# Kernel tuning notes

Hardware: AMD Instinct MI355X
Metric: run time of the kernel (lower is better)

## Reference

```python
import jax, jax.numpy as jnp
import numpy as np

N = 30000      # num nodes
E = 600000     # num edges
D = 128        # feature dim (all layers)
R = 7          # num_relation
G = 16         # num graphs in batch
L = 3          # num layers (hidden_dims = [128,128,128])


def setup_inputs() -> dict:
    key = jax.random.key(0)
    ks = jax.random.split(key, 10)
    x = jax.random.normal(ks[0], (N, D), dtype=jnp.float32)
    node_in = jax.random.randint(ks[1], (E,), 0, N)
    node_out = jax.random.randint(ks[2], (E,), 0, N)
    relation = jax.random.randint(ks[3], (E,), 0, R)
    edge_weight = jax.random.uniform(ks[4], (E,), dtype=jnp.float32)
    node2graph = jnp.sort(jax.random.randint(ks[5], (N,), 0, G))
    # learned params: per-layer relational linear (R*D -> D) and self-loop linear (D -> D)
    Wr = jax.random.normal(ks[6], (L, R * D, D), dtype=jnp.float32) * 0.02
    br = jnp.zeros((L, D), dtype=jnp.float32)
    Wl = jax.random.normal(ks[7], (L, D, D), dtype=jnp.float32) * 0.02
    bl = jnp.zeros((L, D), dtype=jnp.float32)
    return dict(x=x, node_in=node_in, node_out=node_out, relation=relation,
                edge_weight=edge_weight, node2graph=node2graph,
                Wr=Wr, br=br, Wl=Wl, bl=bl)


def reference(x, node_in, node_out, relation, edge_weight, node2graph, Wr, br, Wl, bl):
    # relation-indexed destination segment: node_out * R + relation
    seg = node_out * R + relation            # (E,)
    ew = edge_weight[:, None]                # (E, 1)
    h = x
    for i in range(L):
        msg = h[node_in] * ew                                         # gather + weight, (E, D)
        upd = jax.ops.segment_sum(msg, seg, num_segments=N * R)       # scatter_add, (N*R, D)
        upd = upd.reshape(N, R * D)                                   # per-relation concat
        h = jax.nn.relu(upd @ Wr[i] + br[i] + h @ Wl[i] + bl[i])      # linear + self-loop + act
    node_feature = h                                                  # (N, D)
    graph_feature = jax.ops.segment_sum(node_feature, node2graph, num_segments=G)  # sum readout
    return graph_feature, node_feature
```

## Files before the change

kernel.cpp:

```cpp
#include <hip/hip_runtime.h>

#define NN 30000
#define NE 600000
#define DD 128
#define RR 7
#define GG 16
#define LL 3

typedef short bf16x8 __attribute__((ext_vector_type(8)));
typedef float f32x4  __attribute__((ext_vector_type(4)));

__device__ __forceinline__ unsigned short f2bf(float f) {
    unsigned u = __float_as_uint(f);
    unsigned r = (u + 0x7fffu + ((u >> 16) & 1u)) >> 16;
    return (unsigned short)r;
}

__global__ __launch_bounds__(256) void pack_weights(
    const float* __restrict__ Wl,
    const float* __restrict__ Wr,
    unsigned short* __restrict__ Bw)
{
    int t = blockIdx.x * 256 + threadIdx.x;
    if (t >= LL * 1024 * DD) return;
    int l = t >> 17;
    int rem = t & 131071;
    int n = rem >> 7;
    int k = rem & 127;
    float v;
    if (n < DD) {
        v = Wl[(size_t)l * DD * DD + k * DD + n];
    } else {
        int q = n - DD;
        v = Wr[(size_t)l * RR * DD * DD + (size_t)((q >> 7) * DD + k) * DD + (q & 127)];
    }
    Bw[(size_t)l * 1024 * DD + n * DD + k] = f2bf(v);
}

__global__ __launch_bounds__(256) void convert_bf16(
    const float* __restrict__ in, unsigned short* __restrict__ out, int n4)
{
    int i = blockIdx.x * 256 + threadIdx.x;
    if (i >= n4) return;
    float4 v = ((const float4*)in)[i];
    ushort4 o;
    o.x = f2bf(v.x); o.y = f2bf(v.y); o.z = f2bf(v.z); o.w = f2bf(v.w);
    ((ushort4*)out)[i] = o;
}

#define ASTR 136
__global__ __launch_bounds__(256) void gemm_mfma(
    const unsigned short* __restrict__ hb,
    const unsigned short* __restrict__ Bw,
    const float* __restrict__ br,
    const float* __restrict__ bl,
    float* __restrict__ hacc,
    unsigned short* __restrict__ Zb,
    int N)
{
    __shared__ unsigned short As[64 * ASTR];
    __shared__ unsigned short Bs[128 * ASTR];

    const int tid  = threadIdx.x;
    const int wave = tid >> 6;
    const int lane = tid & 63;
    const int quad = lane >> 4;
    const int l16  = lane & 15;
    const int row0 = blockIdx.x * 64;
    const int col0 = blockIdx.y * 128;

#pragma unroll
    for (int l = 0; l < 4; ++l) {
        int f = tid + l * 256;
        int r = f >> 4;
        int c8 = f & 15;
        int row = row0 + r;
        int4 v = make_int4(0, 0, 0, 0);
        if (row < N) v = *(const int4*)(hb + (size_t)row * DD + c8 * 8);
        *(int4*)(As + r * ASTR + c8 * 8) = v;
    }
#pragma unroll
    for (int l = 0; l < 8; ++l) {
        int f = tid + l * 256;
        int n = f >> 4;
        int c8 = f & 15;
        *(int4*)(Bs + n * ASTR + c8 * 8) =
            *(const int4*)(Bw + (size_t)(col0 + n) * DD + c8 * 8);
    }
    __syncthreads();

    f32x4 acc[4][2];
#pragma unroll
    for (int mt = 0; mt < 4; ++mt)
#pragma unroll
        for (int nt = 0; nt < 2; ++nt)
            acc[mt][nt] = (f32x4){0.f, 0.f, 0.f, 0.f};

    const unsigned short* As_l = As + l16 * ASTR;
    const unsigned short* Bs_l = Bs + (wave * 32 + l16) * ASTR;

#pragma unroll
    for (int kc = 0; kc < 4; ++kc) {
        int ko = kc * 32 + quad * 8;
        bf16x8 a0 = *(const bf16x8*)(As_l + 0 * 16 * ASTR + ko);
        bf16x8 a1 = *(const bf16x8*)(As_l + 1 * 16 * ASTR + ko);
        bf16x8 a2 = *(const bf16x8*)(As_l + 2 * 16 * ASTR + ko);
        bf16x8 a3 = *(const bf16x8*)(As_l + 3 * 16 * ASTR + ko);
        bf16x8 b0 = *(const bf16x8*)(Bs_l + 0 * 16 * ASTR + ko);
        bf16x8 b1 = *(const bf16x8*)(Bs_l + 1 * 16 * ASTR + ko);
        acc[0][0] = __builtin_amdgcn_mfma_f32_16x16x32_bf16(a0, b0, acc[0][0], 0, 0, 0);
        acc[1][0] = __builtin_amdgcn_mfma_f32_16x16x32_bf16(a1, b0, acc[1][0], 0, 0, 0);
        acc[2][0] = __builtin_amdgcn_mfma_f32_16x16x32_bf16(a2, b0, acc[2][0], 0, 0, 0);
        acc[3][0] = __builtin_amdgcn_mfma_f32_16x16x32_bf16(a3, b0, acc[3][0], 0, 0, 0);
        acc[0][1] = __builtin_amdgcn_mfma_f32_16x16x32_bf16(a0, b1, acc[0][1], 0, 0, 0);
        acc[1][1] = __builtin_amdgcn_mfma_f32_16x16x32_bf16(a1, b1, acc[1][1], 0, 0, 0);
        acc[2][1] = __builtin_amdgcn_mfma_f32_16x16x32_bf16(a2, b1, acc[2][1], 0, 0, 0);
        acc[3][1] = __builtin_amdgcn_mfma_f32_16x16x32_bf16(a3, b1, acc[3][1], 0, 0, 0);
    }

    const int ncol = wave * 32 + l16;
    if (col0 == 0) {
        float bias0 = br[ncol] + bl[ncol];
        float bias1 = br[ncol + 16] + bl[ncol + 16];
#pragma unroll
        for (int mt = 0; mt < 4; ++mt) {
#pragma unroll
            for (int reg = 0; reg < 4; ++reg) {
                int row = row0 + mt * 16 + quad * 4 + reg;
                if (row < N) {
                    hacc[(size_t)row * DD + ncol]      = acc[mt][0][reg] + bias0;
                    hacc[(size_t)row * DD + ncol + 16] = acc[mt][1][reg] + bias1;
                }
            }
        }
    } else {
        const int zc = col0 - DD + ncol;
#pragma unroll
        for (int mt = 0; mt < 4; ++mt) {
#pragma unroll
            for (int reg = 0; reg < 4; ++reg) {
                int row = row0 + mt * 16 + quad * 4 + reg;
                if (row < N) {
                    Zb[(size_t)row * (RR * DD) + zc]      = f2bf(acc[mt][0][reg]);
                    Zb[(size_t)row * (RR * DD) + zc + 16] = f2bf(acc[mt][1][reg]);
                }
            }
        }
    }
}

__global__ __launch_bounds__(256) void edge_hist(
    const int* __restrict__ node_out, int* __restrict__ cnt, int E)
{
    int e = blockIdx.x * 256 + threadIdx.x;
    if (e < E) atomicAdd(&cnt[node_out[e]], 1);
}

__global__ __launch_bounds__(256) void scan_blk(
    const int* __restrict__ cnt, int* __restrict__ lscan,
    int* __restrict__ bsum, int N)
{
    __shared__ int s[256];
    int t = threadIdx.x;
    int i = blockIdx.x * 256 + t;
    int v = (i < N) ? cnt[i] : 0;
    s[t] = v;
    __syncthreads();
#pragma unroll
    for (int off = 1; off < 256; off <<= 1) {
        int u = (t >= off) ? s[t - off] : 0;
        __syncthreads();
        s[t] += u;
        __syncthreads();
    }
    if (i < N) lscan[i] = s[t] - v;
    if (t == 255) bsum[blockIdx.x] = s[255];
}

__global__ __launch_bounds__(128) void scan_bsum(
    int* __restrict__ bsum, int* __restrict__ boff, int nb)
{
    __shared__ int s[128];
    int t = threadIdx.x;
    int v = (t < nb) ? bsum[t] : 0;
    s[t] = v;
    __syncthreads();
#pragma unroll
    for (int off = 1; off < 128; off <<= 1) {
        int u = (t >= off) ? s[t - off] : 0;
        __syncthreads();
        s[t] += u;
        __syncthreads();
    }
    if (t < nb) boff[t] = s[t] - v;
}

__global__ __launch_bounds__(256) void scan_add(
    const int* __restrict__ lscan, const int* __restrict__ boff,
    int* __restrict__ start, int* __restrict__ cursor, int N)
{
    int i = blockIdx.x * 256 + threadIdx.x;
    if (i < N) {
        int v = lscan[i] + boff[i >> 8];
        start[i] = v;
        cursor[i] = v;
    }
    if (i == N) start[N] = NE;
}

__global__ __launch_bounds__(256) void edge_scatter_sort(
    const int* __restrict__ node_in,
    const int* __restrict__ node_out,
    const int* __restrict__ relation,
    const float* __restrict__ ew,
    int* __restrict__ cursor,
    int2* __restrict__ meta,
    int E)
{
    int e = blockIdx.x * 256 + threadIdx.x;
    if (e >= E) return;
    int no = node_out[e];
    int pos = atomicAdd(&cursor[no], 1);
    meta[pos] = make_int2(node_in[e] * (RR * DD) + relation[e] * DD,
                          __float_as_int(ew[e]));
}

__global__ __launch_bounds__(256) void aggregate(
    const unsigned short* __restrict__ Zb,
    const int* __restrict__ start,
    const int2* __restrict__ meta,
    const float* __restrict__ hacc,
    float* __restrict__ out_f32,
    unsigned short* __restrict__ out_bf16,
    int N)
{
    int wid = (blockIdx.x * 256 + threadIdx.x) >> 6;
    int lane = threadIdx.x & 63;
    if (wid >= N) return;

    int e0 = start[wid];
    int e1 = start[wid + 1];

    float accx = 0.f, accy = 0.f;
    int e = e0;
    for (; e + 4 <= e1; e += 4) {
        int2 m0 = meta[e + 0];
        int2 m1 = meta[e + 1];
        int2 m2 = meta[e + 2];
        int2 m3 = meta[e + 3];
        unsigned u0 = *(const unsigned*)(Zb + m0.x + lane * 2);
        unsigned u1 = *(const unsigned*)(Zb + m1.x + lane * 2);
        unsigned u2 = *(const unsigned*)(Zb + m2.x + lane * 2);
        unsigned u3 = *(const unsigned*)(Zb + m3.x + lane * 2);
        float w0 = __int_as_float(m0.y), w1 = __int_as_float(m1.y);
        float w2 = __int_as_float(m2.y), w3 = __int_as_float(m3.y);
        accx = fmaf(w0, __uint_as_float(u0 << 16), accx);
        accy = fmaf(w0, __uint_as_float(u0 & 0xffff0000u), accy);
        accx = fmaf(w1, __uint_as_float(u1 << 16), accx);
        accy = fmaf(w1, __uint_as_float(u1 & 0xffff0000u), accy);
        accx = fmaf(w2, __uint_as_float(u2 << 16), accx);
        accy = fmaf(w2, __uint_as_float(u2 & 0xffff0000u), accy);
        accx = fmaf(w3, __uint_as_float(u3 << 16), accx);
        accy = fmaf(w3, __uint_as_float(u3 & 0xffff0000u), accy);
    }
    for (; e < e1; ++e) {
        int2 m = meta[e];
        unsigned u = *(const unsigned*)(Zb + m.x + lane * 2);
        float wt = __int_as_float(m.y);
        accx = fmaf(wt, __uint_as_float(u << 16), accx);
        accy = fmaf(wt, __uint_as_float(u & 0xffff0000u), accy);
    }

    float2 base = *(const float2*)(hacc + (size_t)wid * DD + lane * 2);
    float ox = fmaxf(base.x + accx, 0.f);
    float oy = fmaxf(base.y + accy, 0.f);
    if (out_f32) {
        *(float2*)(out_f32 + (size_t)wid * DD + lane * 2) = make_float2(ox, oy);
    }
    if (out_bf16) {
        ushort2 o; o.x = f2bf(ox); o.y = f2bf(oy);
        *(ushort2*)(out_bf16 + (size_t)wid * DD + lane * 2) = o;
    }
}

__global__ __launch_bounds__(256) void graph_sum(
    const float* __restrict__ nf,
    const int* __restrict__ n2g,
    float* __restrict__ gf,
    int N)
{
    int t = blockIdx.x * 256 + threadIdx.x;
    int chunk = t >> 5;
    int lane = t & 31;
    int n0 = chunk * 16;
    if (n0 >= N) return;
    int nend = n0 + 16; if (nend > N) nend = N;

    float4 acc = make_float4(0.f, 0.f, 0.f, 0.f);
    int curg = n2g[n0];
    for (int n = n0; n < nend; ++n) {
        int g = n2g[n];
        if (g != curg) {
            float* dst = gf + (size_t)curg * DD + lane * 4;
            atomicAdd(dst + 0, acc.x); atomicAdd(dst + 1, acc.y);
            atomicAdd(dst + 2, acc.z); atomicAdd(dst + 3, acc.w);
            acc = make_float4(0.f, 0.f, 0.f, 0.f);
            curg = g;
        }
        float4 v = *(const float4*)(nf + (size_t)n * DD + lane * 4);
        acc.x += v.x; acc.y += v.y; acc.z += v.z; acc.w += v.w;
    }
    float* dst = gf + (size_t)curg * DD + lane * 4;
    atomicAdd(dst + 0, acc.x); atomicAdd(dst + 1, acc.y);
    atomicAdd(dst + 2, acc.z); atomicAdd(dst + 3, acc.w);
}

extern "C" void kernel_launch(void* const* d_in, const int* in_sizes, int n_in,
                              void* d_out, int out_size, void* d_ws, size_t ws_size,
                              hipStream_t stream)
{
    const float* x        = (const float*)d_in[0];
    const int*   node_in  = (const int*)d_in[1];
    const int*   node_out = (const int*)d_in[2];
    const int*   relation = (const int*)d_in[3];
    const float* ew       = (const float*)d_in[4];
    const int*   n2g      = (const int*)d_in[5];
    const float* Wr       = (const float*)d_in[6];
    const float* br       = (const float*)d_in[7];
    const float* Wl       = (const float*)d_in[8];
    const float* bl       = (const float*)d_in[9];

    float* out = (float*)d_out;
    float* gf = out;
    float* nf = out + GG * DD;

    char* w = (char*)d_ws;
    unsigned short* Zb  = (unsigned short*)w;  w += (size_t)NN * RR * DD * 2;
    float* hacc         = (float*)w;           w += (size_t)NN * DD * 4;
    unsigned short* hbA = (unsigned short*)w;  w += (size_t)NN * DD * 2;
    unsigned short* hbB = (unsigned short*)w;  w += (size_t)NN * DD * 2;
    unsigned short* Bw  = (unsigned short*)w;  w += (size_t)LL * 1024 * DD * 2;
    int2*  meta   = (int2*)w;                  w += (size_t)NE * 8;
    int*   start  = (int*)w;                   w += (size_t)(NN + 1) * 4 + 60;
    int*   cursor = (int*)w;                   w += (size_t)NN * 4 + 64;
    int*   cnt    = (int*)w;                   w += (size_t)NN * 4 + 64;
    int*   lscan  = (int*)w;                   w += (size_t)NN * 4 + 64;
    int*   bsum   = (int*)w;                   w += 256 * 4;
    int*   boff   = (int*)w;                   w += 256 * 4;

    const int N = NN, E = NE;
    const int NB = (N + 255) / 256;

    pack_weights<<<(LL * 1024 * DD + 255) / 256, 256, 0, stream>>>(Wl, Wr, Bw);
    convert_bf16<<<(N * DD / 4 + 255) / 256, 256, 0, stream>>>(x, hbA, N * DD / 4);

    hipMemsetAsync(cnt, 0, (size_t)N * sizeof(int), stream);
    edge_hist<<<(E + 255) / 256, 256, 0, stream>>>(node_out, cnt, E);
    scan_blk<<<NB, 256, 0, stream>>>(cnt, lscan, bsum, N);
    scan_bsum<<<1, 128, 0, stream>>>(bsum, boff, NB);
    scan_add<<<(N + 256) / 256, 256, 0, stream>>>(lscan, boff, start, cursor, N);
    edge_scatter_sort<<<(E + 255) / 256, 256, 0, stream>>>(
        node_in, node_out, relation, ew, cursor, meta, E);

    dim3 ggrid((N + 63) / 64, 8);
    unsigned short* hin = hbA;
    unsigned short* hnext = hbB;
    for (int l = 0; l < LL; ++l) {
        const float* br_l = br + (size_t)l * DD;
        const float* bl_l = bl + (size_t)l * DD;
        const unsigned short* Bw_l = Bw + (size_t)l * 1024 * DD;

        gemm_mfma<<<ggrid, 256, 0, stream>>>(hin, Bw_l, br_l, bl_l, hacc, Zb, N);

        bool last = (l == LL - 1);
        aggregate<<<(N * 64 + 255) / 256, 256, 0, stream>>>(
            Zb, start, meta, hacc,
            last ? nf : (float*)nullptr,
            last ? (unsigned short*)nullptr : hnext, N);

        unsigned short* t = hin; hin = hnext; hnext = t;
    }

    hipMemsetAsync(gf, 0, (size_t)GG * DD * sizeof(float), stream);
    int chunks = (N + 15) / 16;
    graph_sum<<<(chunks * 32 + 255) / 256, 256, 0, stream>>>(nf, n2g, gf, N);
}
```

Measured before the change: 353.3 us.

## Use direct global-to-LDS loads in GEMM, bf16 self-loop buffer, wider gather unroll

The GEMM tile loads now use global_load_lds to copy straight into shared memory, which drops the row padding and the bounds guard. The self-loop/bias accumulator is stored as bf16 instead of fp32, halving its write and read traffic. The edge aggregation loop is unrolled to 8 outstanding gathers to add memory-level parallelism. The risks are LDS bank conflicts from the unpadded stride, reduced precision in the residual term, and out-of-range reads on the last row tile.

```diff
diff --git a/kernel.cpp b/kernel.cpp
--- a/kernel.cpp
+++ b/kernel.cpp
@@ -14,6 +14,15 @@
     unsigned u = __float_as_uint(f);
     unsigned r = (u + 0x7fffu + ((u >> 16) & 1u)) >> 16;
     return (unsigned short)r;
+}
+__device__ __forceinline__ float bf2f(unsigned short b) {
+    return __uint_as_float(((unsigned)b) << 16);
+}
+
+__device__ __forceinline__ void gl_lds16(const void* g, void* l) {
+    __builtin_amdgcn_global_load_lds(
+        (const __attribute__((address_space(1))) void*)g,
+        (__attribute__((address_space(3))) void*)l, 16, 0, 0);
 }
 
 __global__ __launch_bounds__(256) void pack_weights(
@@ -48,13 +57,13 @@
     ((ushort4*)out)[i] = o;
 }
 
-#define ASTR 136
+#define ASTR 128
 __global__ __launch_bounds__(256) void gemm_mfma(
     const unsigned short* __restrict__ hb,
     const unsigned short* __restrict__ Bw,
     const float* __restrict__ br,
     const float* __restrict__ bl,
-    float* __restrict__ hacc,
+    unsigned short* __restrict__ haccb,
     unsigned short* __restrict__ Zb,
     int N)
 {
@@ -70,22 +79,16 @@
     const int col0 = blockIdx.y * 128;
 
 #pragma unroll
-    for (int l = 0; l < 4; ++l) {
-        int f = tid + l * 256;
-        int r = f >> 4;
-        int c8 = f & 15;
-        int row = row0 + r;
-        int4 v = make_int4(0, 0, 0, 0);
-        if (row < N) v = *(const int4*)(hb + (size_t)row * DD + c8 * 8);
-        *(int4*)(As + r * ASTR + c8 * 8) = v;
-    }
-#pragma unroll
-    for (int l = 0; l < 8; ++l) {
-        int f = tid + l * 256;
-        int n = f >> 4;
-        int c8 = f & 15;
-        *(int4*)(Bs + n * ASTR + c8 * 8) =
-            *(const int4*)(Bw + (size_t)(col0 + n) * DD + c8 * 8);
+    for (int i = 0; i < 4; ++i) {
+        int g = i * 4 + wave;
+        gl_lds16(hb + (size_t)(row0 + g * 4) * DD + lane * 8,
+                 As + g * 512);
+    }
+#pragma unroll
+    for (int i = 0; i < 8; ++i) {
+        int g = i * 4 + wave;
+        gl_lds16(Bw + (size_t)col0 * DD + (size_t)g * 512 + lane * 8,
+                 Bs + g * 512);
     }
     __syncthreads();
 
@@ -128,8 +131,8 @@
             for (int reg = 0; reg < 4; ++reg) {
                 int row = row0 + mt * 16 + quad * 4 + reg;
                 if (row < N) {
-                    hacc[(size_t)row * DD + ncol]      = acc[mt][0][reg] + bias0;
-                    hacc[(size_t)row * DD + ncol + 16] = acc[mt][1][reg] + bias1;
+                    haccb[(size_t)row * DD + ncol]      = f2bf(acc[mt][0][reg] + bias0);
+                    haccb[(size_t)row * DD + ncol + 16] = f2bf(acc[mt][1][reg] + bias1);
                 }
             }
         }
@@ -229,7 +232,7 @@
     const unsigned short* __restrict__ Zb,
     const int* __restrict__ start,
     const int2* __restrict__ meta,
-    const float* __restrict__ hacc,
+    const unsigned short* __restrict__ haccb,
     float* __restrict__ out_f32,
     unsigned short* __restrict__ out_bf16,
     int N)
@@ -243,27 +246,32 @@
 
     float accx = 0.f, accy = 0.f;
     int e = e0;
-    for (; e + 4 <= e1; e += 4) {
-        int2 m0 = meta[e + 0];
+    for (; e + 8 <= e1; e += 8) {
+        unsigned u[8]; float wt[8];
+#pragma unroll
+        for (int j = 0; j < 8; ++j) {
+            int2 m = meta[e + j];
+            u[j] = *(const unsigned*)(Zb + m.x + lane * 2);
+            wt[j] = __int_as_float(m.y);
+        }
+#pragma unroll
+        for (int j = 0; j < 8; ++j) {
+            accx = fmaf(wt[j], __uint_as_float(u[j] << 16), accx);
+            accy = fmaf(wt[j], __uint_as_float(u[j] & 0xffff0000u), accy);
+        }
+    }
+    for (; e + 2 <= e1; e += 2) {
+        int2 m0 = meta[e];
         int2 m1 = meta[e + 1];
-        int2 m2 = meta[e + 2];
-        int2 m3 = meta[e + 3];
         unsigned u0 = *(const unsigned*)(Zb + m0.x + lane * 2);
         unsigned u1 = *(const unsigned*)(Zb + m1.x + lane * 2);
-        unsigned u2 = *(const unsigned*)(Zb + m2.x + lane * 2);
-        unsigned u3 = *(const unsigned*)(Zb + m3.x + lane * 2);
         float w0 = __int_as_float(m0.y), w1 = __int_as_float(m1.y);
-        float w2 = __int_as_float(m2.y), w3 = __int_as_float(m3.y);
         accx = fmaf(w0, __uint_as_float(u0 << 16), accx);
         accy = fmaf(w0, __uint_as_float(u0 & 0xffff0000u), accy);
         accx = fmaf(w1, __uint_as_float(u1 << 16), accx);
         accy = fmaf(w1, __uint_as_float(u1 & 0xffff0000u), accy);
-        accx = fmaf(w2, __uint_as_float(u2 << 16), accx);
-        accy = fmaf(w2, __uint_as_float(u2 & 0xffff0000u), accy);
-        accx = fmaf(w3, __uint_as_float(u3 << 16), accx);
-        accy = fmaf(w3, __uint_as_float(u3 & 0xffff0000u), accy);
-    }
-    for (; e < e1; ++e) {
+    }
+    if (e < e1) {
         int2 m = meta[e];
         unsigned u = *(const unsigned*)(Zb + m.x + lane * 2);
         float wt = __int_as_float(m.y);
@@ -271,9 +279,9 @@
         accy = fmaf(wt, __uint_as_float(u & 0xffff0000u), accy);
     }
 
-    float2 base = *(const float2*)(hacc + (size_t)wid * DD + lane * 2);
-    float ox = fmaxf(base.x + accx, 0.f);
-    float oy = fmaxf(base.y + accy, 0.f);
+    unsigned bu = *(const unsigned*)(haccb + (size_t)wid * DD + lane * 2);
+    float ox = fmaxf(bf2f((unsigned short)(bu & 0xffffu)) + accx, 0.f);
+    float oy = fmaxf(bf2f((unsigned short)(bu >> 16)) + accy, 0.f);
     if (out_f32) {
         *(float2*)(out_f32 + (size_t)wid * DD + lane * 2) = make_float2(ox, oy);
     }
@@ -335,11 +343,11 @@
     float* nf = out + GG * DD;
 
     char* w = (char*)d_ws;
-    unsigned short* Zb  = (unsigned short*)w;  w += (size_t)NN * RR * DD * 2;
-    float* hacc         = (float*)w;           w += (size_t)NN * DD * 4;
-    unsigned short* hbA = (unsigned short*)w;  w += (size_t)NN * DD * 2;
-    unsigned short* hbB = (unsigned short*)w;  w += (size_t)NN * DD * 2;
-    unsigned short* Bw  = (unsigned short*)w;  w += (size_t)LL * 1024 * DD * 2;
+    unsigned short* Zb   = (unsigned short*)w; w += (size_t)NN * RR * DD * 2;
+    unsigned short* haccb= (unsigned short*)w; w += (size_t)NN * DD * 2;
+    unsigned short* hbA  = (unsigned short*)w; w += (size_t)NN * DD * 2;
+    unsigned short* hbB  = (unsigned short*)w; w += (size_t)NN * DD * 2;
+    unsigned short* Bw   = (unsigned short*)w; w += (size_t)LL * 1024 * DD * 2;
     int2*  meta   = (int2*)w;                  w += (size_t)NE * 8;
     int*   start  = (int*)w;                   w += (size_t)(NN + 1) * 4 + 60;
     int*   cursor = (int*)w;                   w += (size_t)NN * 4 + 64;
@@ -370,11 +378,11 @@
         const float* bl_l = bl + (size_t)l * DD;
         const unsigned short* Bw_l = Bw + (size_t)l * 1024 * DD;
 
-        gemm_mfma<<<ggrid, 256, 0, stream>>>(hin, Bw_l, br_l, bl_l, hacc, Zb, N);
+        gemm_mfma<<<ggrid, 256, 0, stream>>>(hin, Bw_l, br_l, bl_l, haccb, Zb, N);
 
         bool last = (l == LL - 1);
         aggregate<<<(N * 64 + 255) / 256, 256, 0, stream>>>(
-            Zb, start, meta, hacc,
+            Zb, start, meta, haccb,
             last ? nf : (float*)nullptr,
             last ? (unsigned short*)nullptr : hnext, N);
 
```

Result: faster. 346.3 us (-2.0%).
